# Optimization experiments

Measured on AMD Instinct MI355X. Metric: run time of the kernel, lower is better.

## Reference

```python
import jax, jax.numpy as jnp
import numpy as np

D_MODEL = 1024
H = 16
D_K = D_MODEL // H


def setup_inputs() -> dict:
    key = jax.random.key(0)
    ks = jax.random.split(key, 11)
    B, S = 4, 2048
    scale = 1.0 / np.sqrt(D_MODEL)
    inp = {
        "q": jax.random.normal(ks[0], (B, S, D_MODEL), jnp.float32),
        "k": jax.random.normal(ks[1], (B, S, D_MODEL), jnp.float32),
        "v": jax.random.normal(ks[2], (B, S, D_MODEL), jnp.float32),
        "wq": jax.random.normal(ks[3], (D_MODEL, D_MODEL), jnp.float32) * scale,
        "bq": jax.random.normal(ks[4], (D_MODEL,), jnp.float32) * 0.02,
        "wk": jax.random.normal(ks[5], (D_MODEL, D_MODEL), jnp.float32) * scale,
        "bk": jax.random.normal(ks[6], (D_MODEL,), jnp.float32) * 0.02,
        "wv": jax.random.normal(ks[7], (D_MODEL, D_MODEL), jnp.float32) * scale,
        "bv": jax.random.normal(ks[8], (D_MODEL,), jnp.float32) * 0.02,
        "wo": jax.random.normal(ks[9], (D_MODEL, D_MODEL), jnp.float32) * scale,
        "bo": jax.random.normal(ks[10], (D_MODEL,), jnp.float32) * 0.02,
    }
    return inp


def _split_heads(x):
    b, s, d = x.shape
    return x.reshape(b, s, H, D_K).transpose(0, 2, 1, 3)  # b h s k


def reference(q, k, v, wq, bq, wk, bk, wv, bv, wo, bo):
    # linear projections (torch Linear: x @ W^T + b; here weights stored as [in,out])
    qh = _split_heads(q @ wq + bq)
    kh = _split_heads(k @ wk + bk)
    vh = _split_heads(v @ wv + bv)
    scores = jnp.einsum('bhsk,bhtk->bhst', qh, kh) / np.sqrt(D_K)
    attn = jax.nn.softmax(scores, axis=-1)
    wv_ = jnp.einsum('bhst,bhtk->bhsk', attn, vh)
    b, h, s, dk = wv_.shape
    cv = wv_.transpose(0, 2, 1, 3).reshape(b, s, h * dk)
    return cv @ wo + bo
```

## Files before the change

kernel.cpp:

```cpp
#include <hip/hip_runtime.h>


#define DM 1024
#define SQL 2048

typedef __attribute__((ext_vector_type(4))) float floatx4;
typedef __attribute__((ext_vector_type(8))) __bf16 bf16x8;
typedef __attribute__((ext_vector_type(4))) unsigned int uintx4;

#define SW(row, chunk) (((row) << 6) + ((((chunk) ^ ((row) & 7))) << 3))

#define GLD(gaddr, laddr)                                                              \
  __builtin_amdgcn_global_load_lds(                                                    \
      (const __attribute__((address_space(1))) unsigned int*)(gaddr),                  \
      (__attribute__((address_space(3))) unsigned int*)(laddr), 16, 0, 0)

__device__ __forceinline__ unsigned short f2bf(float f) {
  unsigned int u = __float_as_uint(f);
  u += 0x7fffu + ((u >> 16) & 1u);
  return (unsigned short)(u >> 16);
}

__device__ __forceinline__ unsigned int pack_bf(float lo, float hi) {
  unsigned int a = __float_as_uint(lo) + 0x8000u;
  unsigned int b = __float_as_uint(hi) + 0x8000u;
  return __builtin_amdgcn_perm(b, a, 0x07060302u);
}

__global__ __launch_bounds__(256) void transpose4_kernel(
    const float* __restrict__ w0, const float* __restrict__ w1,
    const float* __restrict__ w2, const float* __restrict__ w3,
    unsigned short* __restrict__ t0, unsigned short* __restrict__ t1,
    unsigned short* __restrict__ t2, unsigned short* __restrict__ t3) {
  __shared__ unsigned short t[64][65];
  int z = blockIdx.z;
  const float* W = (z == 0) ? w0 : (z == 1) ? w1 : (z == 2) ? w2 : w3;
  unsigned short* Wt = (z == 0) ? t0 : (z == 1) ? t1 : (z == 2) ? t2 : t3;
  int tid = threadIdx.x;
  int n0 = blockIdx.x * 64, k0 = blockIdx.y * 64;
  for (int u = 0; u < 16; u++) {
    int idx = u * 256 + tid;
    int k = idx >> 6, n = idx & 63;
    t[k][n] = f2bf(W[(size_t)(k0 + k) * DM + n0 + n]);
  }
  __syncthreads();
  for (int u = 0; u < 16; u++) {
    int idx = u * 256 + tid;
    int n = idx >> 6, k = idx & 63;
    Wt[(size_t)(n0 + n) * DM + k0 + k] = t[k][n];
  }
}

__global__ __launch_bounds__(256) void convert3_kernel(
    const float* __restrict__ s0, const float* __restrict__ s1,
    const float* __restrict__ s2, unsigned short* __restrict__ d0,
    unsigned short* __restrict__ d1, unsigned short* __restrict__ d2) {
  int z = blockIdx.y;
  const float* S = (z == 0) ? s0 : (z == 1) ? s1 : s2;
  unsigned short* D = (z == 0) ? d0 : (z == 1) ? d1 : d2;
  int t = blockIdx.x * 256 + threadIdx.x;
  for (int u = 0; u < 8; u++) {
    int i = (u << 18) + t;
    float4 vv = ((const float4*)S)[i];
    uint2 p;
    p.x = pack_bf(vv.x, vv.y);
    p.y = pack_bf(vv.z, vv.w);
    ((uint2*)D)[i] = p;
  }
}

__global__ __launch_bounds__(256) void gemm_qkv_kernel(
    const unsigned short* __restrict__ Aq, const unsigned short* __restrict__ Ak,
    const unsigned short* __restrict__ Av, const unsigned short* __restrict__ wqt,
    const unsigned short* __restrict__ wkt, const unsigned short* __restrict__ wvt,
    const float* __restrict__ bq, const float* __restrict__ bk,
    const float* __restrict__ bv, unsigned short* __restrict__ Qb,
    unsigned short* __restrict__ Kb, unsigned short* __restrict__ VtOut,
    float qscale) {
  __shared__ unsigned short lds_a[128 * 64];
  __shared__ unsigned short lds_b[128 * 64];
  int z = blockIdx.z;
  const unsigned short* A  = (z == 0) ? Aq : (z == 1) ? Ak : Av;
  const unsigned short* Bt = (z == 0) ? wqt : (z == 1) ? wkt : wvt;
  const float* bias = (z == 0) ? bq : (z == 1) ? bk : bv;

  int tid = threadIdx.x;
  int wave = tid >> 6, lane = tid & 63;
  int quad = lane >> 4, c16 = lane & 15;
  int wm = wave & 1, wn = wave >> 1;
  int l8 = lane & 7, r8 = lane >> 3;
  int m0 = blockIdx.y * 128, n0 = blockIdx.x * 128;

  floatx4 acc[4][4];
  const floatx4 fzero = {0.f, 0.f, 0.f, 0.f};
  for (int i = 0; i < 4; i++)
    for (int j = 0; j < 4; j++) acc[i][j] = fzero;

  for (int kt = 0; kt < DM; kt += 64) {
    for (int u = 0; u < 4; u++) {
      int q = wave * 4 + u;
      int row = q * 8 + r8;
      GLD(&A[(size_t)(m0 + row) * DM + kt + l8 * 8], &lds_a[q * 512]);
      GLD(&Bt[(size_t)(n0 + row) * DM + kt + l8 * 8], &lds_b[q * 512]);
    }
    __syncthreads();
    for (int ks = 0; ks < 2; ks++) {
      bf16x8 af[4], bfr[4];
      for (int i = 0; i < 4; i++)
        af[i] = *(const bf16x8*)&lds_a[(wm * 64 + i * 16 + c16) * 64 + ks * 32 + quad * 8];
      for (int j = 0; j < 4; j++)
        bfr[j] = *(const bf16x8*)&lds_b[(wn * 64 + j * 16 + c16) * 64 + ks * 32 + quad * 8];
      for (int i = 0; i < 4; i++)
        for (int j = 0; j < 4; j++)
          acc[i][j] = __builtin_amdgcn_mfma_f32_16x16x32_bf16(af[i], bfr[j], acc[i][j], 0, 0, 0);
    }
    __syncthreads();
  }

  float scale = (z == 0) ? qscale : 1.0f;
  for (int i = 0; i < 4; i++)
    for (int j = 0; j < 4; j++) {
      int gc = n0 + wn * 64 + j * 16 + c16;
      float bvv = bias[gc];
      float val[4];
      for (int r = 0; r < 4; r++) val[r] = (acc[i][j][r] + bvv) * scale;
      int gr0 = m0 + wm * 64 + i * 16 + quad * 4;
      if (z < 2) {
        unsigned short* O = (z == 0) ? Qb : Kb;
        for (int r = 0; r < 4; r++) O[(size_t)(gr0 + r) * DM + gc] = f2bf(val[r]);
      } else {
        int hh = gc >> 6, dd = gc & 63;
        int bidx = gr0 >> 11, srow = gr0 & 2047;
        int s6 = srow & 63;
        int c6 = (s6 & 32) | ((s6 & 8) << 1) | ((s6 & 4) << 1) | ((s6 & 16) >> 2) | (s6 & 3);
        int srowp = (srow & ~63) | c6;
        uint2 pk;
        pk.x = pack_bf(val[0], val[1]);
        pk.y = pack_bf(val[2], val[3]);
        *(uint2*)&VtOut[((size_t)(bidx * 16 + hh) * 64 + dd) * SQL + srowp] = pk;
      }
    }
}

__global__ __launch_bounds__(256) void gemm_out_kernel(
    const unsigned short* __restrict__ A, const unsigned short* __restrict__ Bt,
    const float* __restrict__ bias, float* __restrict__ O) {
  __shared__ unsigned short lds_a[128 * 64];
  __shared__ unsigned short lds_b[128 * 64];
  int tid = threadIdx.x;
  int wave = tid >> 6, lane = tid & 63;
  int quad = lane >> 4, c16 = lane & 15;
  int wm = wave & 1, wn = wave >> 1;
  int l8 = lane & 7, r8 = lane >> 3;
  int m0 = blockIdx.y * 128, n0 = blockIdx.x * 128;

  floatx4 acc[4][4];
  const floatx4 fzero = {0.f, 0.f, 0.f, 0.f};
  for (int i = 0; i < 4; i++)
    for (int j = 0; j < 4; j++) acc[i][j] = fzero;

  for (int kt = 0; kt < DM; kt += 64) {
    for (int u = 0; u < 4; u++) {
      int q = wave * 4 + u;
      int row = q * 8 + r8;
      GLD(&A[(size_t)(m0 + row) * DM + kt + l8 * 8], &lds_a[q * 512]);
      GLD(&Bt[(size_t)(n0 + row) * DM + kt + l8 * 8], &lds_b[q * 512]);
    }
    __syncthreads();
    for (int ks = 0; ks < 2; ks++) {
      bf16x8 af[4], bfr[4];
      for (int i = 0; i < 4; i++)
        af[i] = *(const bf16x8*)&lds_a[(wm * 64 + i * 16 + c16) * 64 + ks * 32 + quad * 8];
      for (int j = 0; j < 4; j++)
        bfr[j] = *(const bf16x8*)&lds_b[(wn * 64 + j * 16 + c16) * 64 + ks * 32 + quad * 8];
      for (int i = 0; i < 4; i++)
        for (int j = 0; j < 4; j++)
          acc[i][j] = __builtin_amdgcn_mfma_f32_16x16x32_bf16(af[i], bfr[j], acc[i][j], 0, 0, 0);
    }
    __syncthreads();
  }

  for (int i = 0; i < 4; i++)
    for (int j = 0; j < 4; j++) {
      int gc = n0 + wn * 64 + j * 16 + c16;
      float bvv = bias[gc];
      int gr0 = m0 + wm * 64 + i * 16 + quad * 4;
      for (int r = 0; r < 4; r++) O[(size_t)(gr0 + r) * DM + gc] = acc[i][j][r] + bvv;
    }
}

__global__ __launch_bounds__(256, 2) void attn_kernel(
    const unsigned short* __restrict__ Qb, const unsigned short* __restrict__ Kb,
    const unsigned short* __restrict__ Vt, unsigned short* __restrict__ Cv) {
  __shared__ unsigned short lds_k[2][64 * 64];
  __shared__ unsigned short lds_v[2][64 * 64];
  int tid = threadIdx.x;
  int wave = tid >> 6, lane = tid & 63;
  int quad = lane >> 4, c16 = lane & 15;
  int bh = blockIdx.x, qt = blockIdx.y;
  int b = bh >> 4, h = bh & 15;

  int sr0 = tid >> 3, sc = tid & 7;
  const unsigned short* kbase = &Kb[(size_t)(b * SQL) * DM + h * 64 + sc * 8];
  const unsigned short* vbase = &Vt[(size_t)(bh * 64) * SQL + sc * 8];

  bf16x8 qf[4][2];
  for (int i = 0; i < 4; i++)
    for (int ks = 0; ks < 2; ks++) {
      int gr = b * SQL + qt * 256 + wave * 64 + i * 16 + c16;
      qf[i][ks] = *(const bf16x8*)&Qb[(size_t)gr * DM + h * 64 + ks * 32 + quad * 8];
    }

  const floatx4 fzero = {0.f, 0.f, 0.f, 0.f};
  floatx4 acc[4][4];
  for (int dt = 0; dt < 4; dt++)
    for (int i = 0; i < 4; i++) acc[dt][i] = fzero;
  float l_[4] = {0.f, 0.f, 0.f, 0.f};

  for (int u = 0; u < 2; u++) {
    int r = sr0 + u * 32;
    *(uint4*)&lds_k[0][SW(r, sc)] = *(const uint4*)&kbase[(size_t)r * DM];
    *(uint4*)&lds_v[0][SW(r, sc)] = *(const uint4*)&vbase[(size_t)r * SQL];
  }
  __syncthreads();

  for (int t = 0; t < 32; t++) {
    int cur = t & 1;
    uint4 kreg[2], vreg[2];
    if (t + 1 < 32) {
      int t1 = (t + 1) * 64;
      for (int u = 0; u < 2; u++) {
        int r = sr0 + u * 32;
        kreg[u] = *(const uint4*)&kbase[(size_t)(t1 + r) * DM];
        vreg[u] = *(const uint4*)&vbase[(size_t)r * SQL + t1];
      }
    }

    floatx4 s[4][4];
    for (int i = 0; i < 4; i++)
      for (int jt = 0; jt < 4; jt++) s[i][jt] = fzero;
    for (int ks = 0; ks < 2; ks++) {
      bf16x8 kf[4];
      for (int jt = 0; jt < 4; jt++)
        kf[jt] = *(const bf16x8*)&lds_k[cur][SW(jt * 16 + c16, ks * 4 + quad)];
      for (int i = 0; i < 4; i++)
        for (int jt = 0; jt < 4; jt++)
          s[i][jt] = __builtin_amdgcn_mfma_f32_16x16x32_bf16(kf[jt], qf[i][ks], s[i][jt], 0, 0, 0);
    }

    uintx4 pw[4][2];
    for (int i = 0; i < 4; i++) {
      float sum = l_[i];
      for (int jt = 0; jt < 4; jt++)
        for (int r = 0; r < 4; r++) {
          float p = __builtin_amdgcn_exp2f(s[i][jt][r]);
          s[i][jt][r] = p;
          sum += p;
        }
      l_[i] = sum;
      for (int ks = 0; ks < 2; ks++) {
        pw[i][ks].x = pack_bf(s[i][2 * ks][0], s[i][2 * ks][1]);
        pw[i][ks].y = pack_bf(s[i][2 * ks][2], s[i][2 * ks][3]);
        pw[i][ks].z = pack_bf(s[i][2 * ks + 1][0], s[i][2 * ks + 1][1]);
        pw[i][ks].w = pack_bf(s[i][2 * ks + 1][2], s[i][2 * ks + 1][3]);
      }
    }

    for (int ks = 0; ks < 2; ks++) {
      for (int dt = 0; dt < 4; dt++) {
        bf16x8 av = *(const bf16x8*)&lds_v[cur][SW(dt * 16 + c16, ks * 4 + quad)];
        for (int i = 0; i < 4; i++)
          acc[dt][i] = __builtin_amdgcn_mfma_f32_16x16x32_bf16(
              av, __builtin_bit_cast(bf16x8, pw[i][ks]), acc[dt][i], 0, 0, 0);
      }
    }

    if (t + 1 < 32) {
      int nxt = cur ^ 1;
      for (int u = 0; u < 2; u++) {
        int r = sr0 + u * 32;
        *(uint4*)&lds_k[nxt][SW(r, sc)] = kreg[u];
        *(uint4*)&lds_v[nxt][SW(r, sc)] = vreg[u];
      }
    }
    __syncthreads();
  }

  for (int i = 0; i < 4; i++) {
    l_[i] += __shfl_xor(l_[i], 16);
    l_[i] += __shfl_xor(l_[i], 32);
    float inv = 1.f / l_[i];
    int gr = b * SQL + qt * 256 + wave * 64 + i * 16 + c16;
    for (int dt = 0; dt < 4; dt++) {
      uint2 pkw;
      pkw.x = pack_bf(acc[dt][i][0] * inv, acc[dt][i][1] * inv);
      pkw.y = pack_bf(acc[dt][i][2] * inv, acc[dt][i][3] * inv);
      *(uint2*)&Cv[(size_t)gr * DM + h * 64 + dt * 16 + quad * 4] = pkw;
    }
  }
}

extern "C" void kernel_launch(void* const* d_in, const int* in_sizes, int n_in,
                              void* d_out, int out_size, void* d_ws, size_t ws_size,
                              hipStream_t stream) {
  const float* q  = (const float*)d_in[0];
  const float* k  = (const float*)d_in[1];
  const float* v  = (const float*)d_in[2];
  const float* wq = (const float*)d_in[3];
  const float* bq = (const float*)d_in[4];
  const float* wk = (const float*)d_in[5];
  const float* bk = (const float*)d_in[6];
  const float* wv = (const float*)d_in[7];
  const float* bv = (const float*)d_in[8];
  const float* wo = (const float*)d_in[9];
  const float* bo = (const float*)d_in[10];
  float* out = (float*)d_out;

  char* ws = (char*)d_ws;
  unsigned short* wqt = (unsigned short*)(ws + (size_t)0);
  unsigned short* wkt = (unsigned short*)(ws + ((size_t)2 << 20));
  unsigned short* wvt = (unsigned short*)(ws + ((size_t)4 << 20));
  unsigned short* wot = (unsigned short*)(ws + ((size_t)6 << 20));
  unsigned short* Qb  = (unsigned short*)(ws + ((size_t)8 << 20));
  unsigned short* Kb  = (unsigned short*)(ws + ((size_t)24 << 20));
  unsigned short* Vt  = (unsigned short*)(ws + ((size_t)40 << 20));
  unsigned short* Cv  = (unsigned short*)(ws + ((size_t)56 << 20));
  unsigned short* Aq = (unsigned short*)d_out;
  unsigned short* Ak = (unsigned short*)d_out + ((size_t)8 << 20);
  unsigned short* Av = Cv;

  const float QSCALE = 0.125f * 1.44269504088896340736f;

  dim3 blk(256);
  transpose4_kernel<<<dim3(16, 16, 4), blk, 0, stream>>>(wq, wk, wv, wo, wqt, wkt, wvt, wot);
  convert3_kernel<<<dim3(1024, 3), blk, 0, stream>>>(q, k, v, Aq, Ak, Av);
  gemm_qkv_kernel<<<dim3(8, 64, 3), blk, 0, stream>>>(Aq, Ak, Av, wqt, wkt, wvt,
                                                      bq, bk, bv, Qb, Kb, Vt, QSCALE);
  attn_kernel<<<dim3(64, 8), blk, 0, stream>>>(Qb, Kb, Vt, Cv);
  gemm_out_kernel<<<dim3(8, 64), blk, 0, stream>>>(Cv, wot, bo, out);
}
```

Before: 347.7 us.

## Rewrite projection GEMMs as 256x128 triple-buffered, swizzled, 512-thread pipelines

Replaces the simple 128x128 load-sync-compute loop in the QKV and output projection GEMMs with a shared 256x128 core run by 8 waves. The core keeps three LDS stages in flight, interleaves global-to-LDS staging with MFMA phases using barriers and s_setprio, and XOR-swizzles LDS rows to avoid bank conflicts. Blocks are remapped so that consecutive blocks share A/B tiles for better L2 reuse. The triple-buffered tiles use about 147KB of LDS per block, so only one block fits per CU, and the extra barriers add sync cost.

```diff
diff --git a/kernel.cpp b/kernel.cpp
--- a/kernel.cpp
+++ b/kernel.cpp
@@ -69,7 +69,133 @@
   }
 }
 
-__global__ __launch_bounds__(256) void gemm_qkv_kernel(
+__device__ __forceinline__ void gemm_core_256x128(
+    const unsigned short* __restrict__ A, const unsigned short* __restrict__ Bt,
+    int m0, int n0, unsigned short* lds_a, unsigned short* lds_b,
+    floatx4 acc[4][4]) {
+  int tid = threadIdx.x;
+  int wave = tid >> 6, lane = tid & 63;
+  int quad = lane >> 4, c16 = lane & 15;
+  int wm = wave >> 1, wn = wave & 1;
+  int r8 = lane >> 3, l8 = lane & 7;
+  int xch = (l8 ^ r8) << 3;
+
+  int r7 = c16 & 7;
+  int aoff0 = ((wm * 64 + c16) << 6) + ((quad ^ r7) << 3);
+  int aoff1 = ((wm * 64 + c16) << 6) + (((4 + quad) ^ r7) << 3);
+  int boff0 = ((wn * 64 + c16) << 6) + ((quad ^ r7) << 3);
+  int boff1 = ((wn * 64 + c16) << 6) + (((4 + quad) ^ r7) << 3);
+
+  int aq = wave * 4;
+  int bq = wave * 2;
+
+#define STG_A(bufp, kt, u) \
+  GLD(&A[(size_t)(m0 + (aq + (u)) * 8 + r8) * DM + (kt) + xch], (bufp) + (aq + (u)) * 512)
+#define STG_B(bufp, kt, u) \
+  GLD(&Bt[(size_t)(n0 + (bq + (u)) * 8 + r8) * DM + (kt) + xch], (bufp) + (bq + (u)) * 512)
+
+  const floatx4 fz = {0.f, 0.f, 0.f, 0.f};
+#pragma unroll
+  for (int i = 0; i < 4; i++)
+#pragma unroll
+    for (int j = 0; j < 4; j++) acc[i][j] = fz;
+
+#pragma unroll
+  for (int u = 0; u < 4; u++) STG_A(lds_a, 0, u);
+  STG_B(lds_b, 0, 0);
+  STG_B(lds_b, 0, 1);
+#pragma unroll
+  for (int u = 0; u < 4; u++) STG_A(lds_a + 16384, 64, u);
+  STG_B(lds_b + 8192, 64, 0);
+  STG_B(lds_b + 8192, 64, 1);
+
+  int cur = 0;
+#pragma unroll 1
+  for (int t = 0; t < 16; ++t) {
+    if (t < 15) asm volatile("s_waitcnt vmcnt(6)\n\ts_barrier" ::: "memory");
+    else        asm volatile("s_waitcnt vmcnt(0)\n\ts_barrier" ::: "memory");
+
+    const unsigned short* la = lds_a + cur * 16384;
+    const unsigned short* lb = lds_b + cur * 8192;
+    int stg = cur + 2;
+    if (stg >= 3) stg -= 3;
+    unsigned short* sa = lds_a + stg * 16384;
+    unsigned short* sb = lds_b + stg * 8192;
+    bool do_st = (t < 14);
+    int kt2 = (t + 2) << 6;
+
+    bf16x8 a_[2], b0[4], b1[4];
+
+    a_[0] = *(const bf16x8*)&la[aoff0];
+    a_[1] = *(const bf16x8*)&la[aoff0 + 1024];
+    b0[0] = *(const bf16x8*)&lb[boff0];
+    b0[1] = *(const bf16x8*)&lb[boff0 + 1024];
+    b0[2] = *(const bf16x8*)&lb[boff0 + 2048];
+    b0[3] = *(const bf16x8*)&lb[boff0 + 3072];
+    if (do_st) { STG_A(sa, kt2, 0); STG_A(sa, kt2, 1); }
+    __builtin_amdgcn_s_barrier();
+    __builtin_amdgcn_s_setprio(1);
+#pragma unroll
+    for (int j = 0; j < 4; j++)
+      acc[0][j] = __builtin_amdgcn_mfma_f32_16x16x32_bf16(a_[0], b0[j], acc[0][j], 0, 0, 0);
+#pragma unroll
+    for (int j = 0; j < 4; j++)
+      acc[1][j] = __builtin_amdgcn_mfma_f32_16x16x32_bf16(a_[1], b0[j], acc[1][j], 0, 0, 0);
+    __builtin_amdgcn_s_setprio(0);
+    __builtin_amdgcn_s_barrier();
+
+    a_[0] = *(const bf16x8*)&la[aoff0 + 2048];
+    a_[1] = *(const bf16x8*)&la[aoff0 + 3072];
+    if (do_st) { STG_A(sa, kt2, 2); STG_A(sa, kt2, 3); }
+    __builtin_amdgcn_s_barrier();
+    __builtin_amdgcn_s_setprio(1);
+#pragma unroll
+    for (int j = 0; j < 4; j++)
+      acc[2][j] = __builtin_amdgcn_mfma_f32_16x16x32_bf16(a_[0], b0[j], acc[2][j], 0, 0, 0);
+#pragma unroll
+    for (int j = 0; j < 4; j++)
+      acc[3][j] = __builtin_amdgcn_mfma_f32_16x16x32_bf16(a_[1], b0[j], acc[3][j], 0, 0, 0);
+    __builtin_amdgcn_s_setprio(0);
+    __builtin_amdgcn_s_barrier();
+
+    a_[0] = *(const bf16x8*)&la[aoff1];
+    a_[1] = *(const bf16x8*)&la[aoff1 + 1024];
+    b1[0] = *(const bf16x8*)&lb[boff1];
+    b1[1] = *(const bf16x8*)&lb[boff1 + 1024];
+    b1[2] = *(const bf16x8*)&lb[boff1 + 2048];
+    b1[3] = *(const bf16x8*)&lb[boff1 + 3072];
+    if (do_st) { STG_B(sb, kt2, 0); STG_B(sb, kt2, 1); }
+    __builtin_amdgcn_s_barrier();
+    __builtin_amdgcn_s_setprio(1);
+#pragma unroll
+    for (int j = 0; j < 4; j++)
+      acc[0][j] = __builtin_amdgcn_mfma_f32_16x16x32_bf16(a_[0], b1[j], acc[0][j], 0, 0, 0);
+#pragma unroll
+    for (int j = 0; j < 4; j++)
+      acc[1][j] = __builtin_amdgcn_mfma_f32_16x16x32_bf16(a_[1], b1[j], acc[1][j], 0, 0, 0);
+    __builtin_amdgcn_s_setprio(0);
+    __builtin_amdgcn_s_barrier();
+
+    a_[0] = *(const bf16x8*)&la[aoff1 + 2048];
+    a_[1] = *(const bf16x8*)&la[aoff1 + 3072];
+    __builtin_amdgcn_s_barrier();
+    __builtin_amdgcn_s_setprio(1);
+#pragma unroll
+    for (int j = 0; j < 4; j++)
+      acc[2][j] = __builtin_amdgcn_mfma_f32_16x16x32_bf16(a_[0], b1[j], acc[2][j], 0, 0, 0);
+#pragma unroll
+    for (int j = 0; j < 4; j++)
+      acc[3][j] = __builtin_amdgcn_mfma_f32_16x16x32_bf16(a_[1], b1[j], acc[3][j], 0, 0, 0);
+    __builtin_amdgcn_s_setprio(0);
+
+    cur = cur + 1;
+    if (cur >= 3) cur = 0;
+  }
+#undef STG_A
+#undef STG_B
+}
+
+__global__ __launch_bounds__(512, 2) void gemm_qkv_kernel(
     const unsigned short* __restrict__ Aq, const unsigned short* __restrict__ Ak,
     const unsigned short* __restrict__ Av, const unsigned short* __restrict__ wqt,
     const unsigned short* __restrict__ wkt, const unsigned short* __restrict__ wvt,
@@ -77,56 +203,41 @@
     const float* __restrict__ bv, unsigned short* __restrict__ Qb,
     unsigned short* __restrict__ Kb, unsigned short* __restrict__ VtOut,
     float qscale) {
-  __shared__ unsigned short lds_a[128 * 64];
-  __shared__ unsigned short lds_b[128 * 64];
-  int z = blockIdx.z;
+  __shared__ unsigned short lds_a[3 * 256 * 64];
+  __shared__ unsigned short lds_b[3 * 128 * 64];
+
+  int lin = blockIdx.x + (blockIdx.y << 3) + (blockIdx.z << 8);
+  int swz = (lin & 7) * 96 + (lin >> 3);
+  int z = swz >> 8, rem = swz & 255;
+  int m0 = (rem >> 3) << 8;
+  int n0 = (rem & 7) << 7;
+
   const unsigned short* A  = (z == 0) ? Aq : (z == 1) ? Ak : Av;
   const unsigned short* Bt = (z == 0) ? wqt : (z == 1) ? wkt : wvt;
   const float* bias = (z == 0) ? bq : (z == 1) ? bk : bv;
 
+  floatx4 acc[4][4];
+  gemm_core_256x128(A, Bt, m0, n0, lds_a, lds_b, acc);
+
   int tid = threadIdx.x;
   int wave = tid >> 6, lane = tid & 63;
   int quad = lane >> 4, c16 = lane & 15;
-  int wm = wave & 1, wn = wave >> 1;
-  int l8 = lane & 7, r8 = lane >> 3;
-  int m0 = blockIdx.y * 128, n0 = blockIdx.x * 128;
-
-  floatx4 acc[4][4];
-  const floatx4 fzero = {0.f, 0.f, 0.f, 0.f};
+  int wm = wave >> 1, wn = wave & 1;
+
+  float scale = (z == 0) ? qscale : 1.0f;
+#pragma unroll
   for (int i = 0; i < 4; i++)
-    for (int j = 0; j < 4; j++) acc[i][j] = fzero;
-
-  for (int kt = 0; kt < DM; kt += 64) {
-    for (int u = 0; u < 4; u++) {
-      int q = wave * 4 + u;
-      int row = q * 8 + r8;
-      GLD(&A[(size_t)(m0 + row) * DM + kt + l8 * 8], &lds_a[q * 512]);
-      GLD(&Bt[(size_t)(n0 + row) * DM + kt + l8 * 8], &lds_b[q * 512]);
-    }
-    __syncthreads();
-    for (int ks = 0; ks < 2; ks++) {
-      bf16x8 af[4], bfr[4];
-      for (int i = 0; i < 4; i++)
-        af[i] = *(const bf16x8*)&lds_a[(wm * 64 + i * 16 + c16) * 64 + ks * 32 + quad * 8];
-      for (int j = 0; j < 4; j++)
-        bfr[j] = *(const bf16x8*)&lds_b[(wn * 64 + j * 16 + c16) * 64 + ks * 32 + quad * 8];
-      for (int i = 0; i < 4; i++)
-        for (int j = 0; j < 4; j++)
-          acc[i][j] = __builtin_amdgcn_mfma_f32_16x16x32_bf16(af[i], bfr[j], acc[i][j], 0, 0, 0);
-    }
-    __syncthreads();
-  }
-
-  float scale = (z == 0) ? qscale : 1.0f;
-  for (int i = 0; i < 4; i++)
+#pragma unroll
     for (int j = 0; j < 4; j++) {
       int gc = n0 + wn * 64 + j * 16 + c16;
       float bvv = bias[gc];
       float val[4];
+#pragma unroll
       for (int r = 0; r < 4; r++) val[r] = (acc[i][j][r] + bvv) * scale;
       int gr0 = m0 + wm * 64 + i * 16 + quad * 4;
       if (z < 2) {
         unsigned short* O = (z == 0) ? Qb : Kb;
+#pragma unroll
         for (int r = 0; r < 4; r++) O[(size_t)(gr0 + r) * DM + gc] = f2bf(val[r]);
       } else {
         int hh = gc >> 6, dd = gc & 63;
@@ -142,49 +253,33 @@
     }
 }
 
-__global__ __launch_bounds__(256) void gemm_out_kernel(
+__global__ __launch_bounds__(512, 2) void gemm_out_kernel(
     const unsigned short* __restrict__ A, const unsigned short* __restrict__ Bt,
     const float* __restrict__ bias, float* __restrict__ O) {
-  __shared__ unsigned short lds_a[128 * 64];
-  __shared__ unsigned short lds_b[128 * 64];
+  __shared__ unsigned short lds_a[3 * 256 * 64];
+  __shared__ unsigned short lds_b[3 * 128 * 64];
+
+  int lin = blockIdx.x + (blockIdx.y << 3);
+  int swz = (lin & 7) * 32 + (lin >> 3);
+  int m0 = (swz >> 3) << 8;
+  int n0 = (swz & 7) << 7;
+
+  floatx4 acc[4][4];
+  gemm_core_256x128(A, Bt, m0, n0, lds_a, lds_b, acc);
+
   int tid = threadIdx.x;
   int wave = tid >> 6, lane = tid & 63;
   int quad = lane >> 4, c16 = lane & 15;
-  int wm = wave & 1, wn = wave >> 1;
-  int l8 = lane & 7, r8 = lane >> 3;
-  int m0 = blockIdx.y * 128, n0 = blockIdx.x * 128;
-
-  floatx4 acc[4][4];
-  const floatx4 fzero = {0.f, 0.f, 0.f, 0.f};
+  int wm = wave >> 1, wn = wave & 1;
+
+#pragma unroll
   for (int i = 0; i < 4; i++)
-    for (int j = 0; j < 4; j++) acc[i][j] = fzero;
-
-  for (int kt = 0; kt < DM; kt += 64) {
-    for (int u = 0; u < 4; u++) {
-      int q = wave * 4 + u;
-      int row = q * 8 + r8;
-      GLD(&A[(size_t)(m0 + row) * DM + kt + l8 * 8], &lds_a[q * 512]);
-      GLD(&Bt[(size_t)(n0 + row) * DM + kt + l8 * 8], &lds_b[q * 512]);
-    }
-    __syncthreads();
-    for (int ks = 0; ks < 2; ks++) {
-      bf16x8 af[4], bfr[4];
-      for (int i = 0; i < 4; i++)
-        af[i] = *(const bf16x8*)&lds_a[(wm * 64 + i * 16 + c16) * 64 + ks * 32 + quad * 8];
-      for (int j = 0; j < 4; j++)
-        bfr[j] = *(const bf16x8*)&lds_b[(wn * 64 + j * 16 + c16) * 64 + ks * 32 + quad * 8];
-      for (int i = 0; i < 4; i++)
-        for (int j = 0; j < 4; j++)
-          acc[i][j] = __builtin_amdgcn_mfma_f32_16x16x32_bf16(af[i], bfr[j], acc[i][j], 0, 0, 0);
-    }
-    __syncthreads();
-  }
-
-  for (int i = 0; i < 4; i++)
+#pragma unroll
     for (int j = 0; j < 4; j++) {
       int gc = n0 + wn * 64 + j * 16 + c16;
       float bvv = bias[gc];
       int gr0 = m0 + wm * 64 + i * 16 + quad * 4;
+#pragma unroll
       for (int r = 0; r < 4; r++) O[(size_t)(gr0 + r) * DM + gc] = acc[i][j][r] + bvv;
     }
 }
@@ -334,8 +429,8 @@
   dim3 blk(256);
   transpose4_kernel<<<dim3(16, 16, 4), blk, 0, stream>>>(wq, wk, wv, wo, wqt, wkt, wvt, wot);
   convert3_kernel<<<dim3(1024, 3), blk, 0, stream>>>(q, k, v, Aq, Ak, Av);
-  gemm_qkv_kernel<<<dim3(8, 64, 3), blk, 0, stream>>>(Aq, Ak, Av, wqt, wkt, wvt,
-                                                      bq, bk, bv, Qb, Kb, Vt, QSCALE);
+  gemm_qkv_kernel<<<dim3(8, 32, 3), dim3(512), 0, stream>>>(Aq, Ak, Av, wqt, wkt, wvt,
+                                                            bq, bk, bv, Qb, Kb, Vt, QSCALE);
   attn_kernel<<<dim3(64, 8), blk, 0, stream>>>(Qb, Kb, Vt, Cv);
-  gemm_out_kernel<<<dim3(8, 64), blk, 0, stream>>>(Cv, wot, bo, out);
-}
+  gemm_out_kernel<<<dim3(8, 32), dim3(512), 0, stream>>>(Cv, wot, bo, out);
+}
```

After: 334.2 us. -3.9%, faster.
